# Kernel tuning notes

Hardware: AMD Instinct MI355X
Metric: run time of the kernel (lower is better)

## Reference

```python
import jax, jax.numpy as jnp
import numpy as np

B, F, N = 128, 256, 2000

def setup_inputs() -> dict:
    key = jax.random.key(0)
    ks = jax.random.split(key, 10)
    s = 0.05
    return {
        'nfeature': jax.random.normal(ks[0], (B, F, N, 1), jnp.float32),
        'last_current': jax.random.randint(ks[1], (B, 2), 0, N, jnp.int32),
        'Wg': jax.random.normal(ks[2], (F, F), jnp.float32) * s,
        'bg': jax.random.normal(ks[3], (F,), jnp.float32) * s,
        'Wnode': jax.random.normal(ks[4], (3 * F, F), jnp.float32) * s,
        'bnode': jax.random.normal(ks[5], (3 * F,), jnp.float32) * s,
        'Wlc': jax.random.normal(ks[6], (F, 2 * F), jnp.float32) * s,
        'blc': jax.random.normal(ks[7], (F,), jnp.float32) * s,
        'Wproj': jax.random.normal(ks[8], (F, F), jnp.float32) * s,
        'bproj': jax.random.normal(ks[9], (F,), jnp.float32) * s,
    }

def reference(nfeature, last_current, Wg, bg, Wnode, bnode, Wlc, blc, Wproj, bproj):
    # nfeature: [B, F, N, 1]
    x = nfeature[..., 0]                                  # [B, F, N]
    f = x.shape[1]
    scale = 1.0 / jnp.sqrt(jnp.asarray(f, x.dtype))
    # global fixed query: max over nodes then Linear
    glb = jnp.max(x, axis=2)                              # [B, F]
    Q = glb @ Wg.T + bg                                   # [B, F]
    # node embeddings via 1x1 conv == channel GEMM, split into K, V, logit_K
    kvl = jnp.einsum('bfn,gf->bgn', x, Wnode) + bnode[None, :, None]  # [B, 3F, N]
    K, V, Klog = jnp.split(kvl, 3, axis=1)                # each [B, F, N]
    # gather last/current city features
    lc = jnp.take_along_axis(x, last_current[:, None, :], axis=2)     # [B, F, 2]
    context = jnp.concatenate([lc[:, :, 0], lc[:, :, 1]], axis=1)     # [B, 2F]
    cQ = context @ Wlc.T + blc + Q                        # [B, F]
    # attention: single query over N keys
    ucj = jnp.einsum('bf,bfn->bn', cQ, K) * scale         # [B, N]
    attn = jax.nn.softmax(ucj, axis=1)
    nc = jnp.einsum('bn,bfn->bf', attn, V)                # [B, F]
    nc = nc @ Wproj.T + bproj                             # [B, F]
    logits = jnp.einsum('bf,bfn->bn', nc, Klog) * scale   # [B, N]
    return jnp.tanh(logits) * 10.0
```

## Files before the change

kernel.cpp:

```cpp
#include <hip/hip_runtime.h>
#include <hip/hip_fp16.h>
#include <math.h>

#define BB 128
#define FF 256
#define NN 2000
#define SW 8
#define SC 256

typedef float f32x4 __attribute__((ext_vector_type(4)));
union H8 { f32x4 v; __half2 h[4]; };

__global__ __launch_bounds__(256) void k_convmax(const float* __restrict__ x,
                                                 __half* __restrict__ xh,
                                                 float* __restrict__ glb) {
    int row  = (blockIdx.x << 2) | (threadIdx.x >> 6);
    int lane = threadIdx.x & 63;
    const f32x4* src = (const f32x4*)(x + (size_t)row * NN);
    f32x4*       dst = (f32x4*)(xh + (size_t)row * NN);
    float m = -INFINITY;
    for (int i = lane; i < 250; i += 64) {
        f32x4 a = __builtin_nontemporal_load(src + 2 * i);
        f32x4 b = __builtin_nontemporal_load(src + 2 * i + 1);
        m = fmaxf(m, fmaxf(fmaxf(a.x, a.y), fmaxf(a.z, a.w)));
        m = fmaxf(m, fmaxf(fmaxf(b.x, b.y), fmaxf(b.z, b.w)));
        H8 o;
        o.h[0] = __floats2half2_rn(a.x, a.y);
        o.h[1] = __floats2half2_rn(a.z, a.w);
        o.h[2] = __floats2half2_rn(b.x, b.y);
        o.h[3] = __floats2half2_rn(b.z, b.w);
        dst[i] = o.v;
    }
#pragma unroll
    for (int off = 32; off; off >>= 1) m = fmaxf(m, __shfl_xor(m, off));
    if (!lane) glb[row] = m;
}

__global__ __launch_bounds__(256) void k_prep(
    const float* __restrict__ x, const int* __restrict__ lc,
    const float* __restrict__ glb,
    const float* __restrict__ Wg, const float* __restrict__ bg,
    const float* __restrict__ Wnode, const float* __restrict__ bnode,
    const float* __restrict__ Wlc, const float* __restrict__ blc,
    float* __restrict__ cK, float* __restrict__ cK0)
{
    int b = blockIdx.x;
    int f = threadIdx.x;
    __shared__ float s_glb[FF], s_ctx[2 * FF], s_cQ[FF], s_red[FF];
    const float* xb = x + (size_t)b * FF * NN;
    s_glb[f] = glb[b * FF + f];
    int l0 = lc[2 * b], l1 = lc[2 * b + 1];
    s_ctx[f]      = xb[(size_t)f * NN + l0];
    s_ctx[FF + f] = xb[(size_t)f * NN + l1];
    __syncthreads();
    const float* wg = Wg + (size_t)f * FF;
    float q0 = 0, q1 = 0, q2 = 0, q3 = 0;
    for (int j = 0; j < FF; j += 4) {
        q0 = fmaf(wg[j],     s_glb[j],     q0);
        q1 = fmaf(wg[j + 1], s_glb[j + 1], q1);
        q2 = fmaf(wg[j + 2], s_glb[j + 2], q2);
        q3 = fmaf(wg[j + 3], s_glb[j + 3], q3);
    }
    const float* wl = Wlc + (size_t)f * 2 * FF;
    for (int j = 0; j < 2 * FF; j += 4) {
        q0 = fmaf(wl[j],     s_ctx[j],     q0);
        q1 = fmaf(wl[j + 1], s_ctx[j + 1], q1);
        q2 = fmaf(wl[j + 2], s_ctx[j + 2], q2);
        q3 = fmaf(wl[j + 3], s_ctx[j + 3], q3);
    }
    float cq = bg[f] + blc[f] + ((q0 + q1) + (q2 + q3));
    s_cQ[f]  = cq;
    s_red[f] = cq * bnode[f];
    __syncthreads();
    float c0 = 0, c1 = 0;
    for (int g = 0; g < FF; g += 2) {
        c0 = fmaf(s_cQ[g],     Wnode[(size_t)g * FF + f],       c0);
        c1 = fmaf(s_cQ[g + 1], Wnode[(size_t)(g + 1) * FF + f], c1);
    }
    cK[b * FF + f] = c0 + c1;
    for (int s = 128; s > 0; s >>= 1) {
        if (f < s) s_red[f] += s_red[f + s];
        __syncthreads();
    }
    if (f == 0) cK0[b] = s_red[0];
}

__global__ __launch_bounds__(512) void k_attn(
    const __half* __restrict__ xh,
    const float* __restrict__ cK, const float* __restrict__ cK0,
    float* __restrict__ y_part, float* __restrict__ m_part,
    float* __restrict__ s_part)
{
    int b = blockIdx.x >> 3, st = blockIdx.x & 7;
    int tid = threadIdx.x, w = tid >> 6, lane = tid & 63;
    int par = lane >> 5, chunk = lane & 31;
    __shared__ __half tile[FF][SC];
    __shared__ float s_u[8][SC];
    __shared__ float s_p[SC];
    __shared__ float s_cK[FF];
    __shared__ float s_red[8], s_red2[8];
    if (tid < FF) s_cK[tid] = cK[b * FF + tid];
    __syncthreads();

    int colbase = (st << 8) + (chunk << 3);
    bool cvalid = colbase < NN;
    const __half* base = xh + ((size_t)(b * FF) + (w << 5) + par) * NN + colbase;

    float up0 = 0, up1 = 0, up2 = 0, up3 = 0, up4 = 0, up5 = 0, up6 = 0, up7 = 0;
#pragma unroll
    for (int g = 0; g < 4; ++g) {
        f32x4 hv[4];
#pragma unroll
        for (int r = 0; r < 4; ++r) {
            if (cvalid) hv[r] = *(const f32x4*)(base + (size_t)((g << 3) + (r << 1)) * NN);
            else        hv[r] = (f32x4){0.f, 0.f, 0.f, 0.f};
        }
#pragma unroll
        for (int r = 0; r < 4; ++r) {
            int row = (w << 5) + par + (g << 3) + (r << 1);
            *(f32x4*)&tile[row][chunk << 3] = hv[r];
            H8 u; u.v = hv[r];
            float c = s_cK[row];
            float2 q0 = __half22float2(u.h[0]);
            float2 q1 = __half22float2(u.h[1]);
            float2 q2 = __half22float2(u.h[2]);
            float2 q3 = __half22float2(u.h[3]);
            up0 = fmaf(c, q0.x, up0); up1 = fmaf(c, q0.y, up1);
            up2 = fmaf(c, q1.x, up2); up3 = fmaf(c, q1.y, up3);
            up4 = fmaf(c, q2.x, up4); up5 = fmaf(c, q2.y, up5);
            up6 = fmaf(c, q3.x, up6); up7 = fmaf(c, q3.y, up7);
        }
    }
    up0 += __shfl_xor(up0, 32); up1 += __shfl_xor(up1, 32);
    up2 += __shfl_xor(up2, 32); up3 += __shfl_xor(up3, 32);
    up4 += __shfl_xor(up4, 32); up5 += __shfl_xor(up5, 32);
    up6 += __shfl_xor(up6, 32); up7 += __shfl_xor(up7, 32);
    if (!par) {
        f32x4 v0 = {up0, up1, up2, up3}, v1 = {up4, up5, up6, up7};
        *(f32x4*)&s_u[w][chunk << 3]       = v0;
        *(f32x4*)&s_u[w][(chunk << 3) + 4] = v1;
    }
    __syncthreads();

    const float scale = 0.0625f;
    float uu = -INFINITY;
    if (tid < SC) {
        int col = (st << 8) + tid;
        if (col < NN) {
            float usum = 0.f;
#pragma unroll
            for (int ww = 0; ww < 8; ++ww) usum += s_u[ww][tid];
            uu = (usum + cK0[b]) * scale;
        }
    }
    float m = uu;
#pragma unroll
    for (int off = 32; off; off >>= 1) m = fmaxf(m, __shfl_xor(m, off));
    if (!lane && w < 4) s_red[w] = m;
    __syncthreads();
    float M = fmaxf(fmaxf(s_red[0], s_red[1]), fmaxf(s_red[2], s_red[3]));
    float e = (uu > -INFINITY) ? __expf(uu - M) : 0.f;
    if (tid < SC) s_p[tid] = e;
    float ssum = e;
#pragma unroll
    for (int off = 32; off; off >>= 1) ssum += __shfl_xor(ssum, off);
    if (!lane && w < 4) s_red2[w] = ssum;
    __syncthreads();
    if (!tid) {
        m_part[(b << 3) + st] = M;
        s_part[(b << 3) + st] = s_red2[0] + s_red2[1] + s_red2[2] + s_red2[3];
    }

    f32x4 pv0 = *(const f32x4*)&s_p[chunk << 3];
    f32x4 pv1 = *(const f32x4*)&s_p[(chunk << 3) + 4];
    float acc[16];
#pragma unroll
    for (int k = 0; k < 16; ++k) {
        int row = (w << 5) + par + (k << 1);
        H8 u; u.v = *(const f32x4*)&tile[row][chunk << 3];
        float2 q0 = __half22float2(u.h[0]);
        float2 q1 = __half22float2(u.h[1]);
        float2 q2 = __half22float2(u.h[2]);
        float2 q3 = __half22float2(u.h[3]);
        float a = 0.f;
        a = fmaf(pv0.x, q0.x, a); a = fmaf(pv0.y, q0.y, a);
        a = fmaf(pv0.z, q1.x, a); a = fmaf(pv0.w, q1.y, a);
        a = fmaf(pv1.x, q2.x, a); a = fmaf(pv1.y, q2.y, a);
        a = fmaf(pv1.z, q3.x, a); a = fmaf(pv1.w, q3.y, a);
        acc[k] = a;
    }
    __syncthreads();
    float* tbuf = (float*)&tile[0][0];
#pragma unroll
    for (int k = 0; k < 16; ++k)
        tbuf[(w << 10) + ((par + (k << 1)) << 5) + chunk] = acc[k];
    __syncthreads();
    {
        int row = tid >> 1, half = tid & 1;
        const float* src = tbuf + ((row >> 5) << 10) + ((row & 31) << 5) + (half << 4);
        f32x4 a0 = *(const f32x4*)src;
        f32x4 a1 = *(const f32x4*)(src + 4);
        f32x4 a2 = *(const f32x4*)(src + 8);
        f32x4 a3 = *(const f32x4*)(src + 12);
        float sm = ((a0.x + a0.y) + (a0.z + a0.w)) + ((a1.x + a1.y) + (a1.z + a1.w)) +
                   ((a2.x + a2.y) + (a2.z + a2.w)) + ((a3.x + a3.y) + (a3.z + a3.w));
        sm += __shfl_xor(sm, 1);
        if (!half) y_part[(size_t)((b << 3) + st) * FF + row] = sm;
    }
}

__global__ __launch_bounds__(256) void k_dense(
    const float* __restrict__ y_part, const float* __restrict__ m_part,
    const float* __restrict__ s_part,
    const float* __restrict__ Wnode, const float* __restrict__ bnode,
    const float* __restrict__ Wproj, const float* __restrict__ bproj,
    float* __restrict__ cL, float* __restrict__ cL0)
{
    int b = blockIdx.x;
    int f = threadIdx.x;
    int wid = f >> 6, lane = f & 63;
    __shared__ float s_y[FF], s_v[FF], s_red[4];

    float M = -INFINITY;
#pragma unroll
    for (int s = 0; s < 8; ++s) M = fmaxf(M, m_part[(b << 3) + s]);
    float S = 0.f, wgt[8];
#pragma unroll
    for (int s = 0; s < 8; ++s) {
        wgt[s] = __expf(m_part[(b << 3) + s] - M);
        S = fmaf(wgt[s], s_part[(b << 3) + s], S);
    }
    float invS = 1.0f / S;
    float acc = 0.f;
#pragma unroll
    for (int s = 0; s < 8; ++s)
        acc = fmaf(wgt[s], y_part[(size_t)((b << 3) + s) * FF + f], acc);
    s_y[f] = acc * invS;
    __syncthreads();

    const float* wv = Wnode + (size_t)(FF + f) * FF;
    float a0 = 0, a1 = 0, a2 = 0, a3 = 0;
    for (int j = 0; j < FF; j += 4) {
        a0 = fmaf(wv[j],     s_y[j],     a0);
        a1 = fmaf(wv[j + 1], s_y[j + 1], a1);
        a2 = fmaf(wv[j + 2], s_y[j + 2], a2);
        a3 = fmaf(wv[j + 3], s_y[j + 3], a3);
    }
    s_v[f] = bnode[FF + f] + ((a0 + a1) + (a2 + a3));
    __syncthreads();
    const float* wp = Wproj + (size_t)f * FF;
    a0 = 0; a1 = 0; a2 = 0; a3 = 0;
    for (int j = 0; j < FF; j += 4) {
        a0 = fmaf(wp[j],     s_v[j],     a0);
        a1 = fmaf(wp[j + 1], s_v[j + 1], a1);
        a2 = fmaf(wp[j + 2], s_v[j + 2], a2);
        a3 = fmaf(wp[j + 3], s_v[j + 3], a3);
    }
    float nc2 = bproj[f] + ((a0 + a1) + (a2 + a3));
    __syncthreads();
    s_v[f] = nc2;
    __syncthreads();
    float c0 = 0, c1 = 0;
    for (int g = 0; g < FF; g += 2) {
        c0 = fmaf(s_v[g],     Wnode[(size_t)(2 * FF + g) * FF + f],     c0);
        c1 = fmaf(s_v[g + 1], Wnode[(size_t)(2 * FF + g + 1) * FF + f], c1);
    }
    cL[b * FF + f] = c0 + c1;
    float t = nc2 * bnode[2 * FF + f];
#pragma unroll
    for (int off = 32; off; off >>= 1) t += __shfl_xor(t, off);
    if (!lane) s_red[wid] = t;
    __syncthreads();
    if (!f) cL0[b] = s_red[0] + s_red[1] + s_red[2] + s_red[3];
}

__global__ __launch_bounds__(512) void k_logits(const __half* __restrict__ xh,
                                                const float* __restrict__ cL,
                                                const float* __restrict__ cL0,
                                                float* __restrict__ out)
{
    int b = blockIdx.x >> 3, st = blockIdx.x & 7;
    int tid = threadIdx.x, w = tid >> 6, lane = tid & 63;
    int par = lane >> 5, chunk = lane & 31;
    __shared__ float s_cL[FF];
    __shared__ float s_acc[8][SC];
    if (tid < FF) s_cL[tid] = cL[b * FF + tid];
    __syncthreads();

    int colbase = (st << 8) + (chunk << 3);
    bool cvalid = colbase < NN;
    const __half* base = xh + ((size_t)(b * FF) + (w << 5) + par) * NN + colbase;
    float up0 = 0, up1 = 0, up2 = 0, up3 = 0, up4 = 0, up5 = 0, up6 = 0, up7 = 0;
    if (cvalid) {
#pragma unroll
        for (int g = 0; g < 4; ++g) {
            f32x4 hv[4];
#pragma unroll
            for (int r = 0; r < 4; ++r)
                hv[r] = *(const f32x4*)(base + (size_t)((g << 3) + (r << 1)) * NN);
#pragma unroll
            for (int r = 0; r < 4; ++r) {
                int row = (w << 5) + par + (g << 3) + (r << 1);
                H8 u; u.v = hv[r];
                float c = s_cL[row];
                float2 q0 = __half22float2(u.h[0]);
                float2 q1 = __half22float2(u.h[1]);
                float2 q2 = __half22float2(u.h[2]);
                float2 q3 = __half22float2(u.h[3]);
                up0 = fmaf(c, q0.x, up0); up1 = fmaf(c, q0.y, up1);
                up2 = fmaf(c, q1.x, up2); up3 = fmaf(c, q1.y, up3);
                up4 = fmaf(c, q2.x, up4); up5 = fmaf(c, q2.y, up5);
                up6 = fmaf(c, q3.x, up6); up7 = fmaf(c, q3.y, up7);
            }
        }
    }
    up0 += __shfl_xor(up0, 32); up1 += __shfl_xor(up1, 32);
    up2 += __shfl_xor(up2, 32); up3 += __shfl_xor(up3, 32);
    up4 += __shfl_xor(up4, 32); up5 += __shfl_xor(up5, 32);
    up6 += __shfl_xor(up6, 32); up7 += __shfl_xor(up7, 32);
    if (!par) {
        f32x4 v0 = {up0, up1, up2, up3}, v1 = {up4, up5, up6, up7};
        *(f32x4*)&s_acc[w][chunk << 3]       = v0;
        *(f32x4*)&s_acc[w][(chunk << 3) + 4] = v1;
    }
    __syncthreads();
    if (tid < SC) {
        int col = (st << 8) + tid;
        if (col < NN) {
            float t = 0.f;
#pragma unroll
            for (int ww = 0; ww < 8; ++ww) t += s_acc[ww][tid];
            out[(size_t)b * NN + col] = tanhf((t + cL0[b]) * 0.0625f) * 10.f;
        }
    }
}

extern "C" void kernel_launch(void* const* d_in, const int* in_sizes, int n_in,
                              void* d_out, int out_size, void* d_ws, size_t ws_size,
                              hipStream_t stream) {
    const float* x     = (const float*)d_in[0];
    const int*   lc    = (const int*)d_in[1];
    const float* Wg    = (const float*)d_in[2];
    const float* bg    = (const float*)d_in[3];
    const float* Wnode = (const float*)d_in[4];
    const float* bnode = (const float*)d_in[5];
    const float* Wlc   = (const float*)d_in[6];
    const float* blc   = (const float*)d_in[7];
    const float* Wproj = (const float*)d_in[8];
    const float* bproj = (const float*)d_in[9];
    float* out = (float*)d_out;

    float* ws     = (float*)d_ws;
    float* glb    = ws + 0;
    float* cK     = ws + 40960;
    float* cK0    = ws + 81920;
    float* m_part = ws + 82944;
    float* s_part = ws + 84992;
    float* cL     = ws + 87040;
    float* cL0    = ws + 120832;
    float* y_part = ws + 121856;
    __half* xh    = (__half*)(ws + (2 << 20));

    k_convmax<<<BB * FF / 4, 256, 0, stream>>>(x, xh, glb);
    k_prep   <<<BB, 256, 0, stream>>>(x, lc, glb, Wg, bg, Wnode, bnode, Wlc, blc, cK, cK0);
    k_attn   <<<BB * SW, 512, 0, stream>>>(xh, cK, cK0, y_part, m_part, s_part);
    k_dense  <<<BB, 256, 0, stream>>>(y_part, m_part, s_part, Wnode, bnode, Wproj, bproj, cL, cL0);
    k_logits <<<BB * SW, 512, 0, stream>>>(xh, cL, cL0, out);
}
```

Baseline: 191.5 us.

## Halve attention column tile, keep tiles in registers, fuse context gather into convmax

Splits the node dimension into 16 column slices of 128 instead of 8 of 256, so the attention and logits kernels launch twice as many blocks. Each thread keeps its loaded fp16 K/V tile in registers and reuses it for the weighted-V pass, which removes the 128 KB shared-memory tile and the extra shared-memory reduction stage. The last/current city gather now happens inside the convert/max pass, so k_prep no longer does strided fp32 loads from x. The tradeoff is more partial results to merge in k_dense and higher register pressure per thread.

Result: slower. 235.8 us (+23.2%).

```diff
diff --git a/kernel.cpp b/kernel.cpp
--- a/kernel.cpp
+++ b/kernel.cpp
@@ -5,30 +5,49 @@
 #define BB 128
 #define FF 256
 #define NN 2000
-#define SW 8
-#define SC 256
+#define NST 16
+#define SC 128
 
 typedef float f32x4 __attribute__((ext_vector_type(4)));
 union H8 { f32x4 v; __half2 h[4]; };
 
+__device__ __forceinline__ float sel8(f32x4 a, f32x4 b, int e) {
+    float v;
+    switch (e) {
+        case 0: v = a.x; break; case 1: v = a.y; break;
+        case 2: v = a.z; break; case 3: v = a.w; break;
+        case 4: v = b.x; break; case 5: v = b.y; break;
+        case 6: v = b.z; break; default: v = b.w; break;
+    }
+    return v;
+}
+
 __global__ __launch_bounds__(256) void k_convmax(const float* __restrict__ x,
+                                                 const int* __restrict__ lc,
                                                  __half* __restrict__ xh,
-                                                 float* __restrict__ glb) {
+                                                 float* __restrict__ glb,
+                                                 float* __restrict__ xg) {
     int row  = (blockIdx.x << 2) | (threadIdx.x >> 6);
     int lane = threadIdx.x & 63;
+    int b    = row >> 8;
+    const int c0 = lc[2 * b], c1 = lc[2 * b + 1];
+    const int i0 = c0 >> 3, e0 = c0 & 7;
+    const int i1 = c1 >> 3, e1 = c1 & 7;
     const f32x4* src = (const f32x4*)(x + (size_t)row * NN);
     f32x4*       dst = (f32x4*)(xh + (size_t)row * NN);
     float m = -INFINITY;
     for (int i = lane; i < 250; i += 64) {
         f32x4 a = __builtin_nontemporal_load(src + 2 * i);
-        f32x4 b = __builtin_nontemporal_load(src + 2 * i + 1);
+        f32x4 q = __builtin_nontemporal_load(src + 2 * i + 1);
         m = fmaxf(m, fmaxf(fmaxf(a.x, a.y), fmaxf(a.z, a.w)));
-        m = fmaxf(m, fmaxf(fmaxf(b.x, b.y), fmaxf(b.z, b.w)));
+        m = fmaxf(m, fmaxf(fmaxf(q.x, q.y), fmaxf(q.z, q.w)));
+        if (i == i0) xg[row * 2]     = sel8(a, q, e0);
+        if (i == i1) xg[row * 2 + 1] = sel8(a, q, e1);
         H8 o;
         o.h[0] = __floats2half2_rn(a.x, a.y);
         o.h[1] = __floats2half2_rn(a.z, a.w);
-        o.h[2] = __floats2half2_rn(b.x, b.y);
-        o.h[3] = __floats2half2_rn(b.z, b.w);
+        o.h[2] = __floats2half2_rn(q.x, q.y);
+        o.h[3] = __floats2half2_rn(q.z, q.w);
         dst[i] = o.v;
     }
 #pragma unroll
@@ -37,8 +56,7 @@
 }
 
 __global__ __launch_bounds__(256) void k_prep(
-    const float* __restrict__ x, const int* __restrict__ lc,
-    const float* __restrict__ glb,
+    const float* __restrict__ xg, const float* __restrict__ glb,
     const float* __restrict__ Wg, const float* __restrict__ bg,
     const float* __restrict__ Wnode, const float* __restrict__ bnode,
     const float* __restrict__ Wlc, const float* __restrict__ blc,
@@ -47,11 +65,10 @@
     int b = blockIdx.x;
     int f = threadIdx.x;
     __shared__ float s_glb[FF], s_ctx[2 * FF], s_cQ[FF], s_red[FF];
-    const float* xb = x + (size_t)b * FF * NN;
     s_glb[f] = glb[b * FF + f];
-    int l0 = lc[2 * b], l1 = lc[2 * b + 1];
-    s_ctx[f]      = xb[(size_t)f * NN + l0];
-    s_ctx[FF + f] = xb[(size_t)f * NN + l1];
+    float2 g2 = ((const float2*)xg)[b * FF + f];
+    s_ctx[f]      = g2.x;
+    s_ctx[FF + f] = g2.y;
     __syncthreads();
     const float* wg = Wg + (size_t)f * FF;
     float q0 = 0, q1 = 0, q2 = 0, q3 = 0;
@@ -91,61 +108,58 @@
     float* __restrict__ y_part, float* __restrict__ m_part,
     float* __restrict__ s_part)
 {
-    int b = blockIdx.x >> 3, st = blockIdx.x & 7;
+    int b = blockIdx.x >> 4, st = blockIdx.x & 15;
     int tid = threadIdx.x, w = tid >> 6, lane = tid & 63;
-    int par = lane >> 5, chunk = lane & 31;
-    __shared__ __half tile[FF][SC];
+    int r2 = lane >> 4, ch = lane & 15;
     __shared__ float s_u[8][SC];
     __shared__ float s_p[SC];
     __shared__ float s_cK[FF];
-    __shared__ float s_red[8], s_red2[8];
+    __shared__ float s_red[4];
     if (tid < FF) s_cK[tid] = cK[b * FF + tid];
     __syncthreads();
 
-    int colbase = (st << 8) + (chunk << 3);
-    bool cvalid = colbase < NN;
-    const __half* base = xh + ((size_t)(b * FF) + (w << 5) + par) * NN + colbase;
-
-    float up0 = 0, up1 = 0, up2 = 0, up3 = 0, up4 = 0, up5 = 0, up6 = 0, up7 = 0;
-#pragma unroll
-    for (int g = 0; g < 4; ++g) {
-        f32x4 hv[4];
-#pragma unroll
-        for (int r = 0; r < 4; ++r) {
-            if (cvalid) hv[r] = *(const f32x4*)(base + (size_t)((g << 3) + (r << 1)) * NN);
-            else        hv[r] = (f32x4){0.f, 0.f, 0.f, 0.f};
-        }
-#pragma unroll
-        for (int r = 0; r < 4; ++r) {
-            int row = (w << 5) + par + (g << 3) + (r << 1);
-            *(f32x4*)&tile[row][chunk << 3] = hv[r];
-            H8 u; u.v = hv[r];
-            float c = s_cK[row];
-            float2 q0 = __half22float2(u.h[0]);
-            float2 q1 = __half22float2(u.h[1]);
-            float2 q2 = __half22float2(u.h[2]);
-            float2 q3 = __half22float2(u.h[3]);
-            up0 = fmaf(c, q0.x, up0); up1 = fmaf(c, q0.y, up1);
-            up2 = fmaf(c, q1.x, up2); up3 = fmaf(c, q1.y, up3);
-            up4 = fmaf(c, q2.x, up4); up5 = fmaf(c, q2.y, up5);
-            up6 = fmaf(c, q3.x, up6); up7 = fmaf(c, q3.y, up7);
-        }
-    }
-    up0 += __shfl_xor(up0, 32); up1 += __shfl_xor(up1, 32);
-    up2 += __shfl_xor(up2, 32); up3 += __shfl_xor(up3, 32);
-    up4 += __shfl_xor(up4, 32); up5 += __shfl_xor(up5, 32);
-    up6 += __shfl_xor(up6, 32); up7 += __shfl_xor(up7, 32);
-    if (!par) {
-        f32x4 v0 = {up0, up1, up2, up3}, v1 = {up4, up5, up6, up7};
-        *(f32x4*)&s_u[w][chunk << 3]       = v0;
-        *(f32x4*)&s_u[w][(chunk << 3) + 4] = v1;
-    }
-    __syncthreads();
-
+    const int colbase = st * SC + (ch << 3);
+    const bool cvalid = colbase < NN;
+    const __half* base = xh + (size_t)(b * FF) * NN + colbase;
     const float scale = 0.0625f;
+
+    f32x4 hv[8];
+#pragma unroll
+    for (int it = 0; it < 8; ++it) {
+        if (cvalid) hv[it] = *(const f32x4*)(base + (size_t)((w << 5) + (it << 2) + r2) * NN);
+        else        hv[it] = (f32x4){0.f, 0.f, 0.f, 0.f};
+    }
+    float uc0 = 0, uc1 = 0, uc2 = 0, uc3 = 0, uc4 = 0, uc5 = 0, uc6 = 0, uc7 = 0;
+#pragma unroll
+    for (int it = 0; it < 8; ++it) {
+        H8 u; u.v = hv[it];
+        float c = s_cK[(w << 5) + (it << 2) + r2];
+        float2 q0 = __half22float2(u.h[0]);
+        float2 q1 = __half22float2(u.h[1]);
+        float2 q2 = __half22float2(u.h[2]);
+        float2 q3 = __half22float2(u.h[3]);
+        uc0 = fmaf(c, q0.x, uc0); uc1 = fmaf(c, q0.y, uc1);
+        uc2 = fmaf(c, q1.x, uc2); uc3 = fmaf(c, q1.y, uc3);
+        uc4 = fmaf(c, q2.x, uc4); uc5 = fmaf(c, q2.y, uc5);
+        uc6 = fmaf(c, q3.x, uc6); uc7 = fmaf(c, q3.y, uc7);
+    }
+    uc0 += __shfl_xor(uc0, 16); uc0 += __shfl_xor(uc0, 32);
+    uc1 += __shfl_xor(uc1, 16); uc1 += __shfl_xor(uc1, 32);
+    uc2 += __shfl_xor(uc2, 16); uc2 += __shfl_xor(uc2, 32);
+    uc3 += __shfl_xor(uc3, 16); uc3 += __shfl_xor(uc3, 32);
+    uc4 += __shfl_xor(uc4, 16); uc4 += __shfl_xor(uc4, 32);
+    uc5 += __shfl_xor(uc5, 16); uc5 += __shfl_xor(uc5, 32);
+    uc6 += __shfl_xor(uc6, 16); uc6 += __shfl_xor(uc6, 32);
+    uc7 += __shfl_xor(uc7, 16); uc7 += __shfl_xor(uc7, 32);
+    if (r2 == 0) {
+        *(f32x4*)&s_u[w][ch << 3]       = (f32x4){uc0, uc1, uc2, uc3};
+        *(f32x4*)&s_u[w][(ch << 3) + 4] = (f32x4){uc4, uc5, uc6, uc7};
+    }
+    __syncthreads();
+
     float uu = -INFINITY;
     if (tid < SC) {
-        int col = (st << 8) + tid;
+        int col = st * SC + tid;
         if (col < NN) {
             float usum = 0.f;
 #pragma unroll
@@ -153,31 +167,30 @@
             uu = (usum + cK0[b]) * scale;
         }
     }
-    float m = uu;
-#pragma unroll
-    for (int off = 32; off; off >>= 1) m = fmaxf(m, __shfl_xor(m, off));
-    if (!lane && w < 4) s_red[w] = m;
-    __syncthreads();
-    float M = fmaxf(fmaxf(s_red[0], s_red[1]), fmaxf(s_red[2], s_red[3]));
+    float mv = uu;
+#pragma unroll
+    for (int off = 32; off; off >>= 1) mv = fmaxf(mv, __shfl_xor(mv, off));
+    if (tid < SC && !lane) s_red[w] = mv;
+    __syncthreads();
+    float M = fmaxf(s_red[0], s_red[1]);
     float e = (uu > -INFINITY) ? __expf(uu - M) : 0.f;
     if (tid < SC) s_p[tid] = e;
-    float ssum = e;
-#pragma unroll
-    for (int off = 32; off; off >>= 1) ssum += __shfl_xor(ssum, off);
-    if (!lane && w < 4) s_red2[w] = ssum;
+    float se = e;
+#pragma unroll
+    for (int off = 32; off; off >>= 1) se += __shfl_xor(se, off);
+    if (tid < SC && !lane) s_red[2 + w] = se;
     __syncthreads();
     if (!tid) {
-        m_part[(b << 3) + st] = M;
-        s_part[(b << 3) + st] = s_red2[0] + s_red2[1] + s_red2[2] + s_red2[3];
-    }
-
-    f32x4 pv0 = *(const f32x4*)&s_p[chunk << 3];
-    f32x4 pv1 = *(const f32x4*)&s_p[(chunk << 3) + 4];
-    float acc[16];
-#pragma unroll
-    for (int k = 0; k < 16; ++k) {
-        int row = (w << 5) + par + (k << 1);
-        H8 u; u.v = *(const f32x4*)&tile[row][chunk << 3];
+        m_part[b * NST + st] = M;
+        s_part[b * NST + st] = s_red[2] + s_red[3];
+    }
+
+    f32x4 pv0 = *(const f32x4*)&s_p[ch << 3];
+    f32x4 pv1 = *(const f32x4*)&s_p[(ch << 3) + 4];
+    float acc[8];
+#pragma unroll
+    for (int it = 0; it < 8; ++it) {
+        H8 u; u.v = hv[it];
         float2 q0 = __half22float2(u.h[0]);
         float2 q1 = __half22float2(u.h[1]);
         float2 q2 = __half22float2(u.h[2]);
@@ -187,25 +200,20 @@
         a = fmaf(pv0.z, q1.x, a); a = fmaf(pv0.w, q1.y, a);
         a = fmaf(pv1.x, q2.x, a); a = fmaf(pv1.y, q2.y, a);
         a = fmaf(pv1.z, q3.x, a); a = fmaf(pv1.w, q3.y, a);
-        acc[k] = a;
-    }
-    __syncthreads();
-    float* tbuf = (float*)&tile[0][0];
-#pragma unroll
-    for (int k = 0; k < 16; ++k)
-        tbuf[(w << 10) + ((par + (k << 1)) << 5) + chunk] = acc[k];
-    __syncthreads();
-    {
-        int row = tid >> 1, half = tid & 1;
-        const float* src = tbuf + ((row >> 5) << 10) + ((row & 31) << 5) + (half << 4);
-        f32x4 a0 = *(const f32x4*)src;
-        f32x4 a1 = *(const f32x4*)(src + 4);
-        f32x4 a2 = *(const f32x4*)(src + 8);
-        f32x4 a3 = *(const f32x4*)(src + 12);
-        float sm = ((a0.x + a0.y) + (a0.z + a0.w)) + ((a1.x + a1.y) + (a1.z + a1.w)) +
-                   ((a2.x + a2.y) + (a2.z + a2.w)) + ((a3.x + a3.y) + (a3.z + a3.w));
-        sm += __shfl_xor(sm, 1);
-        if (!half) y_part[(size_t)((b << 3) + st) * FF + row] = sm;
+        acc[it] = a;
+    }
+#pragma unroll
+    for (int it = 0; it < 8; ++it) {
+        float a = acc[it];
+        a += __shfl_xor(a, 1); a += __shfl_xor(a, 2);
+        a += __shfl_xor(a, 4); a += __shfl_xor(a, 8);
+        acc[it] = a;
+    }
+    if (ch == 0) {
+        float* yp = y_part + (size_t)(b * NST + st) * FF;
+#pragma unroll
+        for (int it = 0; it < 8; ++it)
+            yp[(w << 5) + (it << 2) + r2] = acc[it];
     }
 }
 
@@ -223,18 +231,18 @@
 
     float M = -INFINITY;
 #pragma unroll
-    for (int s = 0; s < 8; ++s) M = fmaxf(M, m_part[(b << 3) + s]);
-    float S = 0.f, wgt[8];
-#pragma unroll
-    for (int s = 0; s < 8; ++s) {
-        wgt[s] = __expf(m_part[(b << 3) + s] - M);
-        S = fmaf(wgt[s], s_part[(b << 3) + s], S);
+    for (int s = 0; s < NST; ++s) M = fmaxf(M, m_part[b * NST + s]);
+    float S = 0.f, wgt[NST];
+#pragma unroll
+    for (int s = 0; s < NST; ++s) {
+        wgt[s] = __expf(m_part[b * NST + s] - M);
+        S = fmaf(wgt[s], s_part[b * NST + s], S);
     }
     float invS = 1.0f / S;
     float acc = 0.f;
 #pragma unroll
-    for (int s = 0; s < 8; ++s)
-        acc = fmaf(wgt[s], y_part[(size_t)((b << 3) + s) * FF + f], acc);
+    for (int s = 0; s < NST; ++s)
+        acc = fmaf(wgt[s], y_part[(size_t)(b * NST + s) * FF + f], acc);
     s_y[f] = acc * invS;
     __syncthreads();
 
@@ -279,57 +287,57 @@
                                                 const float* __restrict__ cL0,
                                                 float* __restrict__ out)
 {
-    int b = blockIdx.x >> 3, st = blockIdx.x & 7;
+    int b = blockIdx.x >> 4, st = blockIdx.x & 15;
     int tid = threadIdx.x, w = tid >> 6, lane = tid & 63;
-    int par = lane >> 5, chunk = lane & 31;
+    int r2 = lane >> 4, ch = lane & 15;
+    __shared__ float s_u[8][SC];
     __shared__ float s_cL[FF];
-    __shared__ float s_acc[8][SC];
     if (tid < FF) s_cL[tid] = cL[b * FF + tid];
     __syncthreads();
 
-    int colbase = (st << 8) + (chunk << 3);
-    bool cvalid = colbase < NN;
-    const __half* base = xh + ((size_t)(b * FF) + (w << 5) + par) * NN + colbase;
-    float up0 = 0, up1 = 0, up2 = 0, up3 = 0, up4 = 0, up5 = 0, up6 = 0, up7 = 0;
-    if (cvalid) {
-#pragma unroll
-        for (int g = 0; g < 4; ++g) {
-            f32x4 hv[4];
-#pragma unroll
-            for (int r = 0; r < 4; ++r)
-                hv[r] = *(const f32x4*)(base + (size_t)((g << 3) + (r << 1)) * NN);
-#pragma unroll
-            for (int r = 0; r < 4; ++r) {
-                int row = (w << 5) + par + (g << 3) + (r << 1);
-                H8 u; u.v = hv[r];
-                float c = s_cL[row];
-                float2 q0 = __half22float2(u.h[0]);
-                float2 q1 = __half22float2(u.h[1]);
-                float2 q2 = __half22float2(u.h[2]);
-                float2 q3 = __half22float2(u.h[3]);
-                up0 = fmaf(c, q0.x, up0); up1 = fmaf(c, q0.y, up1);
-                up2 = fmaf(c, q1.x, up2); up3 = fmaf(c, q1.y, up3);
-                up4 = fmaf(c, q2.x, up4); up5 = fmaf(c, q2.y, up5);
-                up6 = fmaf(c, q3.x, up6); up7 = fmaf(c, q3.y, up7);
-            }
-        }
-    }
-    up0 += __shfl_xor(up0, 32); up1 += __shfl_xor(up1, 32);
-    up2 += __shfl_xor(up2, 32); up3 += __shfl_xor(up3, 32);
-    up4 += __shfl_xor(up4, 32); up5 += __shfl_xor(up5, 32);
-    up6 += __shfl_xor(up6, 32); up7 += __shfl_xor(up7, 32);
-    if (!par) {
-        f32x4 v0 = {up0, up1, up2, up3}, v1 = {up4, up5, up6, up7};
-        *(f32x4*)&s_acc[w][chunk << 3]       = v0;
-        *(f32x4*)&s_acc[w][(chunk << 3) + 4] = v1;
+    const int colbase = st * SC + (ch << 3);
+    const bool cvalid = colbase < NN;
+    const __half* base = xh + (size_t)(b * FF) * NN + colbase;
+
+    f32x4 hv[8];
+#pragma unroll
+    for (int it = 0; it < 8; ++it) {
+        if (cvalid) hv[it] = *(const f32x4*)(base + (size_t)((w << 5) + (it << 2) + r2) * NN);
+        else        hv[it] = (f32x4){0.f, 0.f, 0.f, 0.f};
+    }
+    float uc0 = 0, uc1 = 0, uc2 = 0, uc3 = 0, uc4 = 0, uc5 = 0, uc6 = 0, uc7 = 0;
+#pragma unroll
+    for (int it = 0; it < 8; ++it) {
+        H8 u; u.v = hv[it];
+        float c = s_cL[(w << 5) + (it << 2) + r2];
+        float2 q0 = __half22float2(u.h[0]);
+        float2 q1 = __half22float2(u.h[1]);
+        float2 q2 = __half22float2(u.h[2]);
+        float2 q3 = __half22float2(u.h[3]);
+        uc0 = fmaf(c, q0.x, uc0); uc1 = fmaf(c, q0.y, uc1);
+        uc2 = fmaf(c, q1.x, uc2); uc3 = fmaf(c, q1.y, uc3);
+        uc4 = fmaf(c, q2.x, uc4); uc5 = fmaf(c, q2.y, uc5);
+        uc6 = fmaf(c, q3.x, uc6); uc7 = fmaf(c, q3.y, uc7);
+    }
+    uc0 += __shfl_xor(uc0, 16); uc0 += __shfl_xor(uc0, 32);
+    uc1 += __shfl_xor(uc1, 16); uc1 += __shfl_xor(uc1, 32);
+    uc2 += __shfl_xor(uc2, 16); uc2 += __shfl_xor(uc2, 32);
+    uc3 += __shfl_xor(uc3, 16); uc3 += __shfl_xor(uc3, 32);
+    uc4 += __shfl_xor(uc4, 16); uc4 += __shfl_xor(uc4, 32);
+    uc5 += __shfl_xor(uc5, 16); uc5 += __shfl_xor(uc5, 32);
+    uc6 += __shfl_xor(uc6, 16); uc6 += __shfl_xor(uc6, 32);
+    uc7 += __shfl_xor(uc7, 16); uc7 += __shfl_xor(uc7, 32);
+    if (r2 == 0) {
+        *(f32x4*)&s_u[w][ch << 3]       = (f32x4){uc0, uc1, uc2, uc3};
+        *(f32x4*)&s_u[w][(ch << 3) + 4] = (f32x4){uc4, uc5, uc6, uc7};
     }
     __syncthreads();
     if (tid < SC) {
-        int col = (st << 8) + tid;
+        int col = st * SC + tid;
         if (col < NN) {
             float t = 0.f;
 #pragma unroll
-            for (int ww = 0; ww < 8; ++ww) t += s_acc[ww][tid];
+            for (int ww = 0; ww < 8; ++ww) t += s_u[ww][tid];
             out[(size_t)b * NN + col] = tanhf((t + cL0[b]) * 0.0625f) * 10.f;
         }
     }
@@ -352,18 +360,19 @@
 
     float* ws     = (float*)d_ws;
     float* glb    = ws + 0;
-    float* cK     = ws + 40960;
-    float* cK0    = ws + 81920;
-    float* m_part = ws + 82944;
-    float* s_part = ws + 84992;
-    float* cL     = ws + 87040;
-    float* cL0    = ws + 120832;
-    float* y_part = ws + 121856;
+    float* xg     = ws + 32768;
+    float* cK     = ws + 98304;
+    float* cK0    = ws + 131072;
+    float* m_part = ws + 132096;
+    float* s_part = ws + 134144;
+    float* cL     = ws + 136192;
+    float* cL0    = ws + 168960;
+    float* y_part = ws + 169984;
     __half* xh    = (__half*)(ws + (2 << 20));
 
-    k_convmax<<<BB * FF / 4, 256, 0, stream>>>(x, xh, glb);
-    k_prep   <<<BB, 256, 0, stream>>>(x, lc, glb, Wg, bg, Wnode, bnode, Wlc, blc, cK, cK0);
-    k_attn   <<<BB * SW, 512, 0, stream>>>(xh, cK, cK0, y_part, m_part, s_part);
+    k_convmax<<<BB * FF / 4, 256, 0, stream>>>(x, lc, xh, glb, xg);
+    k_prep   <<<BB, 256, 0, stream>>>(xg, glb, Wg, bg, Wnode, bnode, Wlc, blc, cK, cK0);
+    k_attn   <<<BB * NST, 512, 0, stream>>>(xh, cK, cK0, y_part, m_part, s_part);
     k_dense  <<<BB, 256, 0, stream>>>(y_part, m_part, s_part, Wnode, bnode, Wproj, bproj, cL, cL0);
-    k_logits <<<BB * SW, 512, 0, stream>>>(xh, cL, cL0, out);
-}
+    k_logits <<<BB * NST, 512, 0, stream>>>(xh, cL, cL0, out);
+}
```

## Gather last/current features during convert pass and swizzle LDS tile

Applied to the files above, without the earlier changes.

The fp32-to-fp16 conversion kernel now also captures the two gathered node columns per row as it streams x, writing them to a small workspace buffer. The prep kernel then reads those values instead of doing strided scattered reads from the large fp32 input. Separately, the attention kernel's shared-memory tile indexing is XOR-swizzled by row to reduce LDS bank conflicts. This adds per-iteration compare branches in the streaming loop and shifts the workspace layout.

Result: no change. 193.8 us (+1.2%).

```diff
diff --git a/kernel.cpp b/kernel.cpp
--- a/kernel.cpp
+++ b/kernel.cpp
@@ -11,24 +11,43 @@
 typedef float f32x4 __attribute__((ext_vector_type(4)));
 union H8 { f32x4 v; __half2 h[4]; };
 
+__device__ __forceinline__ float sel8(f32x4 a, f32x4 b, int e) {
+    float v;
+    switch (e) {
+        case 0: v = a.x; break; case 1: v = a.y; break;
+        case 2: v = a.z; break; case 3: v = a.w; break;
+        case 4: v = b.x; break; case 5: v = b.y; break;
+        case 6: v = b.z; break; default: v = b.w; break;
+    }
+    return v;
+}
+
 __global__ __launch_bounds__(256) void k_convmax(const float* __restrict__ x,
+                                                 const int* __restrict__ lc,
                                                  __half* __restrict__ xh,
-                                                 float* __restrict__ glb) {
+                                                 float* __restrict__ glb,
+                                                 float* __restrict__ xg) {
     int row  = (blockIdx.x << 2) | (threadIdx.x >> 6);
     int lane = threadIdx.x & 63;
+    int b    = row >> 8;
+    const int c0 = lc[2 * b], c1 = lc[2 * b + 1];
+    const int i0 = c0 >> 3, e0 = c0 & 7;
+    const int i1 = c1 >> 3, e1 = c1 & 7;
     const f32x4* src = (const f32x4*)(x + (size_t)row * NN);
     f32x4*       dst = (f32x4*)(xh + (size_t)row * NN);
     float m = -INFINITY;
     for (int i = lane; i < 250; i += 64) {
         f32x4 a = __builtin_nontemporal_load(src + 2 * i);
-        f32x4 b = __builtin_nontemporal_load(src + 2 * i + 1);
+        f32x4 q = __builtin_nontemporal_load(src + 2 * i + 1);
         m = fmaxf(m, fmaxf(fmaxf(a.x, a.y), fmaxf(a.z, a.w)));
-        m = fmaxf(m, fmaxf(fmaxf(b.x, b.y), fmaxf(b.z, b.w)));
+        m = fmaxf(m, fmaxf(fmaxf(q.x, q.y), fmaxf(q.z, q.w)));
+        if (i == i0) xg[row * 2]     = sel8(a, q, e0);
+        if (i == i1) xg[row * 2 + 1] = sel8(a, q, e1);
         H8 o;
         o.h[0] = __floats2half2_rn(a.x, a.y);
         o.h[1] = __floats2half2_rn(a.z, a.w);
-        o.h[2] = __floats2half2_rn(b.x, b.y);
-        o.h[3] = __floats2half2_rn(b.z, b.w);
+        o.h[2] = __floats2half2_rn(q.x, q.y);
+        o.h[3] = __floats2half2_rn(q.z, q.w);
         dst[i] = o.v;
     }
 #pragma unroll
@@ -37,8 +56,7 @@
 }
 
 __global__ __launch_bounds__(256) void k_prep(
-    const float* __restrict__ x, const int* __restrict__ lc,
-    const float* __restrict__ glb,
+    const float* __restrict__ xg, const float* __restrict__ glb,
     const float* __restrict__ Wg, const float* __restrict__ bg,
     const float* __restrict__ Wnode, const float* __restrict__ bnode,
     const float* __restrict__ Wlc, const float* __restrict__ blc,
@@ -47,11 +65,10 @@
     int b = blockIdx.x;
     int f = threadIdx.x;
     __shared__ float s_glb[FF], s_ctx[2 * FF], s_cQ[FF], s_red[FF];
-    const float* xb = x + (size_t)b * FF * NN;
     s_glb[f] = glb[b * FF + f];
-    int l0 = lc[2 * b], l1 = lc[2 * b + 1];
-    s_ctx[f]      = xb[(size_t)f * NN + l0];
-    s_ctx[FF + f] = xb[(size_t)f * NN + l1];
+    float2 g2 = ((const float2*)xg)[b * FF + f];
+    s_ctx[f]      = g2.x;
+    s_ctx[FF + f] = g2.y;
     __syncthreads();
     const float* wg = Wg + (size_t)f * FF;
     float q0 = 0, q1 = 0, q2 = 0, q3 = 0;
@@ -118,7 +135,7 @@
 #pragma unroll
         for (int r = 0; r < 4; ++r) {
             int row = (w << 5) + par + (g << 3) + (r << 1);
-            *(f32x4*)&tile[row][chunk << 3] = hv[r];
+            *(f32x4*)&tile[row][(chunk ^ (row & 7)) << 3] = hv[r];
             H8 u; u.v = hv[r];
             float c = s_cK[row];
             float2 q0 = __half22float2(u.h[0]);
@@ -177,7 +194,7 @@
 #pragma unroll
     for (int k = 0; k < 16; ++k) {
         int row = (w << 5) + par + (k << 1);
-        H8 u; u.v = *(const f32x4*)&tile[row][chunk << 3];
+        H8 u; u.v = *(const f32x4*)&tile[row][(chunk ^ (row & 7)) << 3];
         float2 q0 = __half22float2(u.h[0]);
         float2 q1 = __half22float2(u.h[1]);
         float2 q2 = __half22float2(u.h[2]);
@@ -352,17 +369,18 @@
 
     float* ws     = (float*)d_ws;
     float* glb    = ws + 0;
-    float* cK     = ws + 40960;
-    float* cK0    = ws + 81920;
-    float* m_part = ws + 82944;
-    float* s_part = ws + 84992;
-    float* cL     = ws + 87040;
-    float* cL0    = ws + 120832;
-    float* y_part = ws + 121856;
+    float* xg     = ws + 32768;
+    float* cK     = ws + 98304;
+    float* cK0    = ws + 131072;
+    float* m_part = ws + 132096;
+    float* s_part = ws + 134144;
+    float* cL     = ws + 136192;
+    float* cL0    = ws + 168960;
+    float* y_part = ws + 169984;
     __half* xh    = (__half*)(ws + (2 << 20));
 
-    k_convmax<<<BB * FF / 4, 256, 0, stream>>>(x, xh, glb);
-    k_prep   <<<BB, 256, 0, stream>>>(x, lc, glb, Wg, bg, Wnode, bnode, Wlc, blc, cK, cK0);
+    k_convmax<<<BB * FF / 4, 256, 0, stream>>>(x, lc, xh, glb, xg);
+    k_prep   <<<BB, 256, 0, stream>>>(xg, glb, Wg, bg, Wnode, bnode, Wlc, blc, cK, cK0);
     k_attn   <<<BB * SW, 512, 0, stream>>>(xh, cK, cK0, y_part, m_part, s_part);
     k_dense  <<<BB, 256, 0, stream>>>(y_part, m_part, s_part, Wnode, bnode, Wproj, bproj, cL, cL0);
     k_logits <<<BB * SW, 512, 0, stream>>>(xh, cL, cL0, out);
```
